# Kernel tuning notes

Measured on AMD Instinct MI355X. Metric: run time of the kernel, lower is better.

Reference implementation:

```python
import jax, jax.numpy as jnp
import numpy as np

PAD = 50
CLUSTERING_WEIGHT = 1.0
SAMPLE_NUMBER = 8192
EPS = 1e-6


def setup_inputs() -> dict:
    key = jax.random.key(0)
    k1, k2 = jax.random.split(key)
    n, c, h, w = 2, 19, 512, 512
    output = jax.random.uniform(k1, (n, c, h, w), dtype=jnp.float32)
    hw_cropped = (h - 2 * PAD) * (w - 2 * PAD)  # 412*412 = 169744
    sample = jax.random.randint(k2, (SAMPLE_NUMBER,), 0, hw_cropped, dtype=jnp.int64)
    return {"output": output, "sample": sample}


def reference(output, sample):
    n, c, h, w = output.shape
    # crop pad border
    out = output[:, :, PAD:h - PAD, PAD:w - PAD]  # [n, c, h', w']
    prob = out.reshape(n, c, -1)[:, :, sample]     # [n, c, S]
    prob_t = jnp.swapaxes(prob, 1, 2)              # [n, S, c]
    # sampled similarity: [n, S, S] (memory-heavy intermediate)
    sim = jnp.einsum('nsc,ntc->nst', prob_t, prob_t)
    ind = jnp.argmax(sim, axis=2)                  # [n, S]
    # nearest[b, i, k] = prob_t[b, ind[b, i], k]
    nearest = jnp.take_along_axis(prob_t, ind[:, :, None], axis=1)  # [n, S, c]
    # robust_crossentropy(pred=prob_t, tgt=nearest)
    loss = -(nearest * jnp.log(prob_t + EPS))
    loss = loss.mean() * CLUSTERING_WEIGHT
    return loss[None]  # shape [1]
```

## Files before the change

### kernel.cpp

```cpp
#include <hip/hip_runtime.h>
#include <math.h>

#define N 2
#define C 19
#define H 512
#define W 512
#define PADC 50
#define WC 412
#define S 8192
#define CP 20
#define XP 64
#define NCHUNK 16
#define CHUNKT (S / NCHUNK)
#define TTS 128
#define NSTG (CHUNKT / TTS)
#define TPS (TTS / 32)
#define LPITCH 72
#define EPSF 1e-6f

typedef __attribute__((ext_vector_type(8))) short short8;
typedef __attribute__((ext_vector_type(16))) float f32x16;

__device__ __forceinline__ unsigned short f2bf_rne(float x) {
    unsigned u = __float_as_uint(x);
    unsigned r = (u + 0x7FFFu + ((u >> 16) & 1u)) >> 16;
    return (unsigned short)r;
}
__device__ __forceinline__ float bf2f(unsigned short h) {
    return __uint_as_float(((unsigned)h) << 16);
}
__device__ __forceinline__ float max16(const f32x16 a) {
    float m0 = fmaxf(a[0], a[1]),   m1 = fmaxf(a[2], a[3]);
    float m2 = fmaxf(a[4], a[5]),   m3 = fmaxf(a[6], a[7]);
    float m4 = fmaxf(a[8], a[9]),   m5 = fmaxf(a[10], a[11]);
    float m6 = fmaxf(a[12], a[13]), m7 = fmaxf(a[14], a[15]);
    m0 = fmaxf(m0, m1); m2 = fmaxf(m2, m3);
    m4 = fmaxf(m4, m5); m6 = fmaxf(m6, m7);
    m0 = fmaxf(m0, m2); m4 = fmaxf(m4, m6);
    return fmaxf(m0, m4);
}

__global__ void gather_k(const float* __restrict__ out4d,
                         const int* __restrict__ sample,
                         float* __restrict__ P32,
                         unsigned short* __restrict__ X) {
    int idx = blockIdx.x * blockDim.x + threadIdx.x;
    int lane = idx & 31;
    int ns = idx >> 5;
    int nn = ns >> 13;
    int s  = ns & (S - 1);
    int smp = sample[s];
    int row = smp / WC;
    int col = smp - row * WC;
    const float* base = out4d + ((size_t)nn * C) * H * W
                      + (size_t)(PADC + row) * W + (PADC + col);
    float v = 0.f;
    if (lane < C) v = base[(size_t)lane * (H * W)];
    unsigned short hb = f2bf_rne(v);
    float hf = bf2f(hb);
    unsigned short lb = f2bf_rne(v - hf);

    if (lane < CP) P32[(size_t)ns * CP + lane] = v;
    unsigned short* xr = X + (size_t)ns * XP;
    xr[lane]      = hb;
    xr[32 + lane] = lb;
}

__global__ __launch_bounds__(512, 4) void argmax_k(const unsigned short* __restrict__ X,
                                                   unsigned* __restrict__ keys) {
    __shared__ unsigned short lds[2][TTS * LPITCH];
    int b = blockIdx.x;
    int chunk  = b & (NCHUNK - 1);
    int sgroup = (b >> 4) & 15;
    int nn     = b >> 8;
    int tid  = threadIdx.x;
    int w    = tid >> 6;
    int lane = tid & 63;
    int col  = lane & 31;
    int hi   = lane >> 5;
    int s0   = (sgroup * 16 + w) * 32;
    int s1   = s0 + 256;
    int t0   = chunk * CHUNKT;
    const unsigned short* Xn = X + (size_t)nn * S * XP;

    short8 bfA[4], bfB[4];
    {
        const unsigned short* ba = Xn + (size_t)(s0 + col) * XP + hi * 8;
        bfA[0] = *(const short8*)(ba);      bfA[1] = *(const short8*)(ba + 16);
        bfA[2] = *(const short8*)(ba + 32); bfA[3] = *(const short8*)(ba + 48);
        const unsigned short* bb = Xn + (size_t)(s1 + col) * XP + hi * 8;
        bfB[0] = *(const short8*)(bb);      bfB[1] = *(const short8*)(bb + 16);
        bfB[2] = *(const short8*)(bb + 32); bfB[3] = *(const short8*)(bb + 48);
    }

    f32x16 zacc = {};
    unsigned kA = 0u, kB = 0u;

    int r0 = tid >> 3, j0 = tid & 7;
    int r1 = r0 + 64;

    {
        const float4* src = (const float4*)(Xn + (size_t)t0 * XP);
        *(float4*)(&lds[0][r0 * LPITCH + j0 * 8]) = src[tid];
        *(float4*)(&lds[0][r1 * LPITCH + j0 * 8]) = src[tid + 512];
    }
    __syncthreads();

    int cur = 0;
    for (int st = 0; st < NSTG; ++st) {
        float4 na, nb;
        if (st + 1 < NSTG) {
            const float4* srcn = (const float4*)(Xn + (size_t)(t0 + (st + 1) * TTS) * XP);
            na = srcn[tid]; nb = srcn[tid + 512];
        }
        const unsigned short* bs = &lds[cur][0];
        #pragma unroll
        for (int ts = 0; ts < TPS; ++ts) {
            const unsigned short* arow = bs + (ts * 32 + col) * LPITCH + hi * 8;
            short8 a0 = *(const short8*)(arow);
            short8 a1 = *(const short8*)(arow + 16);
            short8 a2 = *(const short8*)(arow + 32);
            short8 a3 = *(const short8*)(arow + 48);
            f32x16 accA = __builtin_amdgcn_mfma_f32_32x32x16_bf16(a0, bfA[0], zacc, 0, 0, 0);
            accA = __builtin_amdgcn_mfma_f32_32x32x16_bf16(a1, bfA[1], accA, 0, 0, 0);
            accA = __builtin_amdgcn_mfma_f32_32x32x16_bf16(a0, bfA[2], accA, 0, 0, 0);
            accA = __builtin_amdgcn_mfma_f32_32x32x16_bf16(a1, bfA[3], accA, 0, 0, 0);
            accA = __builtin_amdgcn_mfma_f32_32x32x16_bf16(a2, bfA[0], accA, 0, 0, 0);
            accA = __builtin_amdgcn_mfma_f32_32x32x16_bf16(a3, bfA[1], accA, 0, 0, 0);
            f32x16 accB = __builtin_amdgcn_mfma_f32_32x32x16_bf16(a0, bfB[0], zacc, 0, 0, 0);
            accB = __builtin_amdgcn_mfma_f32_32x32x16_bf16(a1, bfB[1], accB, 0, 0, 0);
            accB = __builtin_amdgcn_mfma_f32_32x32x16_bf16(a0, bfB[2], accB, 0, 0, 0);
            accB = __builtin_amdgcn_mfma_f32_32x32x16_bf16(a1, bfB[3], accB, 0, 0, 0);
            accB = __builtin_amdgcn_mfma_f32_32x32x16_bf16(a2, bfB[0], accB, 0, 0, 0);
            accB = __builtin_amdgcn_mfma_f32_32x32x16_bf16(a3, bfB[1], accB, 0, 0, 0);
            int tile = st * TPS + ts;
            unsigned tb = (unsigned)(63 - tile);
            float mA = fmaxf(max16(accA), 0.f);
            float mB = fmaxf(max16(accB), 0.f);
            unsigned vA = (__float_as_uint(mA) & ~63u) | tb;
            unsigned vB = (__float_as_uint(mB) & ~63u) | tb;
            kA = kA > vA ? kA : vA;
            kB = kB > vB ? kB : vB;
        }
        if (st + 1 < NSTG) {
            *(float4*)(&lds[cur ^ 1][r0 * LPITCH + j0 * 8]) = na;
            *(float4*)(&lds[cur ^ 1][r1 * LPITCH + j0 * 8]) = nb;
        }
        __syncthreads();
        cur ^= 1;
    }

    unsigned oA = __shfl(kA, lane ^ 32, 64);
    unsigned oB = __shfl(kB, lane ^ 32, 64);
    kA = kA > oA ? kA : oA;
    kB = kB > oB ? kB : oB;
    if (lane < 32) {
        size_t basek = ((size_t)nn * NCHUNK + chunk) * S;
        keys[basek + s0 + col] = kA;
        keys[basek + s1 + col] = kB;
    }
}

__global__ __launch_bounds__(256) void refine_k(const float* __restrict__ P32,
                                                const unsigned* __restrict__ keys,
                                                int* __restrict__ ind) {
    int tid = threadIdx.x;
    int wv = blockIdx.x * 4 + (tid >> 6);
    int lane = tid & 63;
    int hi = lane >> 5;
    int l  = lane & 31;
    int ns = wv * 2 + hi;
    int nn = ns >> 13;
    int s  = ns & (S - 1);

    const unsigned* kp = keys + (size_t)nn * NCHUNK * S + s;
    unsigned bk = kp[0]; int bc = 0;
    #pragma unroll
    for (int c = 1; c < NCHUNK; ++c) {
        unsigned k = kp[(size_t)c * S];
        if ((k >> 6) > (bk >> 6)) { bk = k; bc = c; }
    }
    int tile = 63 - (int)(bk & 63u);
    int tbase = bc * CHUNKT + tile * 32;

    const float* Pn = P32 + (size_t)nn * S * CP;
    const float* sr = Pn + (size_t)s * CP;
    const float* tr = Pn + (size_t)(tbase + l) * CP;
    float v = 0.f;
    #pragma unroll
    for (int c = 0; c < C; ++c) v = fmaf(sr[c], tr[c], v);
    int t = tbase + l;
    #pragma unroll
    for (int off = 16; off > 0; off >>= 1) {
        float ov = __shfl_xor(v, off, 32);
        int   ot = __shfl_xor(t, off, 32);
        if (ov > v || (ov == v && ot < t)) { v = ov; t = ot; }
    }
    if (l == 0) ind[ns] = t;
}

__global__ __launch_bounds__(256) void loss_k(const float* __restrict__ P32,
                                              const int* __restrict__ ind,
                                              float* __restrict__ bsum) {
    __shared__ float red[256];
    int idx = blockIdx.x * 256 + threadIdx.x;
    int nn = idx >> 13;
    int s  = idx & (S - 1);
    int bi = ind[idx];

    const float* Pn   = P32 + (size_t)nn * S * CP;
    const float* nrow = Pn + (size_t)bi * CP;
    const float* ps   = Pn + (size_t)s  * CP;
    float acc = 0.f;
    #pragma unroll
    for (int c = 0; c < C; ++c) acc -= nrow[c] * logf(ps[c] + EPSF);

    red[threadIdx.x] = acc;
    __syncthreads();
    for (int off = 128; off > 0; off >>= 1) {
        if (threadIdx.x < off) red[threadIdx.x] += red[threadIdx.x + off];
        __syncthreads();
    }
    if (threadIdx.x == 0) bsum[blockIdx.x] = red[0];
}

__global__ void final_k(const float* __restrict__ bsum, float* __restrict__ out) {
    float t = 0.f;
    for (int i = 0; i < (N * S) / 256; ++i) t += bsum[i];
    out[0] = t / (float)(N * S * C);
}

extern "C" void kernel_launch(void* const* d_in, const int* in_sizes, int n_in,
                              void* d_out, int out_size, void* d_ws, size_t ws_size,
                              hipStream_t stream) {
    const float* out4d  = (const float*)d_in[0];
    const int*   sample = (const int*)d_in[1];

    float*          P32  = (float*)d_ws;
    unsigned short* X    = (unsigned short*)(P32 + (size_t)N * S * CP);
    unsigned*       keys = (unsigned*)(X + (size_t)N * S * XP);
    int*            ind  = (int*)(keys + (size_t)N * NCHUNK * S);
    float*          bsum = (float*)(ind + (size_t)N * S);
    float*          outp = (float*)d_out;

    gather_k<<<(N * S * 32) / 256, 256, 0, stream>>>(out4d, sample, P32, X);
    argmax_k<<<N * 16 * NCHUNK, 512, 0, stream>>>(X, keys);
    refine_k<<<(N * S) / 8, 256, 0, stream>>>(P32, keys, ind);
    loss_k<<<(N * S) / 256, 256, 0, stream>>>(P32, ind, bsum);
    final_k<<<1, 1, 0, stream>>>(bsum, outp);
}
```

Before: 43.06 us.

## Pack split-bf16 operands to halve MFMAs, fuse refine with loss, parallelize final reduce

The gather kernel now writes two asymmetric packed operand layouts, so the hi*hi, hi*lo and lo*hi products of the split-bf16 dot product fit into 4 MFMAs per tile instead of 6. This cuts matrix-core work in the dominant argmax kernel. The refine and loss kernels are merged so the nearest index never goes through global memory, and the single-thread final sum becomes a 256-thread block reduction. The new packing depends on exact channel-slot arithmetic, so any slot mismatch would silently change the similarity values.

```diff
diff --git a/kernel.cpp b/kernel.cpp
--- a/kernel.cpp
+++ b/kernel.cpp
@@ -29,23 +29,26 @@
 __device__ __forceinline__ float bf2f(unsigned short h) {
     return __uint_as_float(((unsigned)h) << 16);
 }
-__device__ __forceinline__ float max16(const f32x16 a) {
-    float m0 = fmaxf(a[0], a[1]),   m1 = fmaxf(a[2], a[3]);
-    float m2 = fmaxf(a[4], a[5]),   m3 = fmaxf(a[6], a[7]);
-    float m4 = fmaxf(a[8], a[9]),   m5 = fmaxf(a[10], a[11]);
-    float m6 = fmaxf(a[12], a[13]), m7 = fmaxf(a[14], a[15]);
-    m0 = fmaxf(m0, m1); m2 = fmaxf(m2, m3);
-    m4 = fmaxf(m4, m5); m6 = fmaxf(m6, m7);
-    m0 = fmaxf(m0, m2); m4 = fmaxf(m4, m6);
-    return fmaxf(m0, m4);
+__device__ __forceinline__ float max16c(const f32x16 a) {
+    float m0 = fmaxf(fmaxf(a[0], a[1]), a[2]);
+    float m1 = fmaxf(fmaxf(a[3], a[4]), a[5]);
+    float m2 = fmaxf(fmaxf(a[6], a[7]), a[8]);
+    float m3 = fmaxf(fmaxf(a[9], a[10]), a[11]);
+    float m4 = fmaxf(fmaxf(a[12], a[13]), a[14]);
+    float n0 = fmaxf(fmaxf(m0, m1), m2);
+    float n1 = fmaxf(fmaxf(m3, m4), a[15]);
+    return fmaxf(fmaxf(n0, n1), 0.f);
 }
 
 __global__ void gather_k(const float* __restrict__ out4d,
                          const int* __restrict__ sample,
                          float* __restrict__ P32,
-                         unsigned short* __restrict__ X) {
+                         unsigned short* __restrict__ XA,
+                         unsigned short* __restrict__ XB) {
     int idx = blockIdx.x * blockDim.x + threadIdx.x;
-    int lane = idx & 31;
+    int lane = idx & 63;
+    int hi   = lane >> 5;
+    int l    = lane & 31;
     int ns = idx >> 5;
     int nn = ns >> 13;
     int s  = ns & (S - 1);
@@ -55,18 +58,35 @@
     const float* base = out4d + ((size_t)nn * C) * H * W
                       + (size_t)(PADC + row) * W + (PADC + col);
     float v = 0.f;
-    if (lane < C) v = base[(size_t)lane * (H * W)];
-    unsigned short hb = f2bf_rne(v);
-    float hf = bf2f(hb);
-    unsigned short lb = f2bf_rne(v - hf);
-
-    if (lane < CP) P32[(size_t)ns * CP + lane] = v;
-    unsigned short* xr = X + (size_t)ns * XP;
-    xr[lane]      = hb;
-    xr[32 + lane] = lb;
-}
-
-__global__ __launch_bounds__(512, 4) void argmax_k(const unsigned short* __restrict__ X,
+    if (l < C) v = base[(size_t)l * (H * W)];
+    unsigned hb = f2bf_rne(v);
+    unsigned lb = f2bf_rne(v - bf2f((unsigned short)hb));
+
+    if (l < CP) P32[(size_t)ns * CP + l] = v;
+
+    int base32 = hi << 5;
+    int srcA = base32 + (l < C ? l : l - C);
+    int srcB = base32 + (l < C ? l : l - 6);
+    unsigned lbA = (unsigned)__shfl((int)lb, srcA, 64);
+    unsigned hbA = (unsigned)__shfl((int)hb, srcA, 64);
+    unsigned lbB = (unsigned)__shfl((int)lb, srcB, 64);
+    unsigned hbB = (unsigned)__shfl((int)hb, srcB, 64);
+
+    unsigned short a0 = (unsigned short)(l < C ? hb : lbA);
+    unsigned short a1 = (unsigned short)(l < C ? hb : (l < 25 ? lbB : 0u));
+    unsigned short b0 = (unsigned short)hbA;
+    unsigned short b1 = (unsigned short)(l < C ? lb : (l < 25 ? hbB : 0u));
+
+    unsigned short* xa = XA + (size_t)ns * XP;
+    unsigned short* xb = XB + (size_t)ns * XP;
+    xa[l]      = a0;
+    xa[32 + l] = a1;
+    xb[l]      = b0;
+    xb[32 + l] = b1;
+}
+
+__global__ __launch_bounds__(512, 4) void argmax_k(const unsigned short* __restrict__ XA,
+                                                   const unsigned short* __restrict__ XB,
                                                    unsigned* __restrict__ keys) {
     __shared__ unsigned short lds[2][TTS * LPITCH];
     int b = blockIdx.x;
@@ -81,14 +101,15 @@
     int s0   = (sgroup * 16 + w) * 32;
     int s1   = s0 + 256;
     int t0   = chunk * CHUNKT;
-    const unsigned short* Xn = X + (size_t)nn * S * XP;
+    const unsigned short* XAn = XA + (size_t)nn * S * XP;
+    const unsigned short* XBn = XB + (size_t)nn * S * XP;
 
     short8 bfA[4], bfB[4];
     {
-        const unsigned short* ba = Xn + (size_t)(s0 + col) * XP + hi * 8;
+        const unsigned short* ba = XBn + (size_t)(s0 + col) * XP + hi * 8;
         bfA[0] = *(const short8*)(ba);      bfA[1] = *(const short8*)(ba + 16);
         bfA[2] = *(const short8*)(ba + 32); bfA[3] = *(const short8*)(ba + 48);
-        const unsigned short* bb = Xn + (size_t)(s1 + col) * XP + hi * 8;
+        const unsigned short* bb = XBn + (size_t)(s1 + col) * XP + hi * 8;
         bfB[0] = *(const short8*)(bb);      bfB[1] = *(const short8*)(bb + 16);
         bfB[2] = *(const short8*)(bb + 32); bfB[3] = *(const short8*)(bb + 48);
     }
@@ -100,7 +121,7 @@
     int r1 = r0 + 64;
 
     {
-        const float4* src = (const float4*)(Xn + (size_t)t0 * XP);
+        const float4* src = (const float4*)(XAn + (size_t)t0 * XP);
         *(float4*)(&lds[0][r0 * LPITCH + j0 * 8]) = src[tid];
         *(float4*)(&lds[0][r1 * LPITCH + j0 * 8]) = src[tid + 512];
     }
@@ -110,7 +131,7 @@
     for (int st = 0; st < NSTG; ++st) {
         float4 na, nb;
         if (st + 1 < NSTG) {
-            const float4* srcn = (const float4*)(Xn + (size_t)(t0 + (st + 1) * TTS) * XP);
+            const float4* srcn = (const float4*)(XAn + (size_t)(t0 + (st + 1) * TTS) * XP);
             na = srcn[tid]; nb = srcn[tid + 512];
         }
         const unsigned short* bs = &lds[cur][0];
@@ -123,22 +144,16 @@
             short8 a3 = *(const short8*)(arow + 48);
             f32x16 accA = __builtin_amdgcn_mfma_f32_32x32x16_bf16(a0, bfA[0], zacc, 0, 0, 0);
             accA = __builtin_amdgcn_mfma_f32_32x32x16_bf16(a1, bfA[1], accA, 0, 0, 0);
-            accA = __builtin_amdgcn_mfma_f32_32x32x16_bf16(a0, bfA[2], accA, 0, 0, 0);
-            accA = __builtin_amdgcn_mfma_f32_32x32x16_bf16(a1, bfA[3], accA, 0, 0, 0);
-            accA = __builtin_amdgcn_mfma_f32_32x32x16_bf16(a2, bfA[0], accA, 0, 0, 0);
-            accA = __builtin_amdgcn_mfma_f32_32x32x16_bf16(a3, bfA[1], accA, 0, 0, 0);
+            accA = __builtin_amdgcn_mfma_f32_32x32x16_bf16(a2, bfA[2], accA, 0, 0, 0);
+            accA = __builtin_amdgcn_mfma_f32_32x32x16_bf16(a3, bfA[3], accA, 0, 0, 0);
             f32x16 accB = __builtin_amdgcn_mfma_f32_32x32x16_bf16(a0, bfB[0], zacc, 0, 0, 0);
             accB = __builtin_amdgcn_mfma_f32_32x32x16_bf16(a1, bfB[1], accB, 0, 0, 0);
-            accB = __builtin_amdgcn_mfma_f32_32x32x16_bf16(a0, bfB[2], accB, 0, 0, 0);
-            accB = __builtin_amdgcn_mfma_f32_32x32x16_bf16(a1, bfB[3], accB, 0, 0, 0);
-            accB = __builtin_amdgcn_mfma_f32_32x32x16_bf16(a2, bfB[0], accB, 0, 0, 0);
-            accB = __builtin_amdgcn_mfma_f32_32x32x16_bf16(a3, bfB[1], accB, 0, 0, 0);
+            accB = __builtin_amdgcn_mfma_f32_32x32x16_bf16(a2, bfB[2], accB, 0, 0, 0);
+            accB = __builtin_amdgcn_mfma_f32_32x32x16_bf16(a3, bfB[3], accB, 0, 0, 0);
             int tile = st * TPS + ts;
             unsigned tb = (unsigned)(63 - tile);
-            float mA = fmaxf(max16(accA), 0.f);
-            float mB = fmaxf(max16(accB), 0.f);
-            unsigned vA = (__float_as_uint(mA) & ~63u) | tb;
-            unsigned vB = (__float_as_uint(mB) & ~63u) | tb;
+            unsigned vA = (__float_as_uint(max16c(accA)) & ~63u) | tb;
+            unsigned vB = (__float_as_uint(max16c(accB)) & ~63u) | tb;
             kA = kA > vA ? kA : vA;
             kB = kB > vB ? kB : vB;
         }
@@ -161,15 +176,15 @@
     }
 }
 
-__global__ __launch_bounds__(256) void refine_k(const float* __restrict__ P32,
-                                                const unsigned* __restrict__ keys,
-                                                int* __restrict__ ind) {
+__global__ __launch_bounds__(256) void refine_loss_k(const float* __restrict__ P32,
+                                                     const unsigned* __restrict__ keys,
+                                                     float* __restrict__ bsum) {
+    __shared__ float red[8];
     int tid = threadIdx.x;
-    int wv = blockIdx.x * 4 + (tid >> 6);
     int lane = tid & 63;
     int hi = lane >> 5;
     int l  = lane & 31;
-    int ns = wv * 2 + hi;
+    int ns = blockIdx.x * 8 + (tid >> 6) * 2 + hi;
     int nn = ns >> 13;
     int s  = ns & (S - 1);
 
@@ -196,38 +211,36 @@
         int   ot = __shfl_xor(t, off, 32);
         if (ov > v || (ov == v && ot < t)) { v = ov; t = ot; }
     }
-    if (l == 0) ind[ns] = t;
-}
-
-__global__ __launch_bounds__(256) void loss_k(const float* __restrict__ P32,
-                                              const int* __restrict__ ind,
-                                              float* __restrict__ bsum) {
+    const float* nrow = Pn + (size_t)t * CP;
+    float term = 0.f;
+    if (l < C) term = -nrow[l] * logf(sr[l] + EPSF);
+    #pragma unroll
+    for (int off = 16; off > 0; off >>= 1)
+        term += __shfl_xor(term, off, 32);
+    if (l == 0) red[tid >> 5] = term;
+    __syncthreads();
+    if (tid == 0) {
+        float a = 0.f;
+        #pragma unroll
+        for (int i = 0; i < 8; ++i) a += red[i];
+        bsum[blockIdx.x] = a;
+    }
+}
+
+__global__ __launch_bounds__(256) void final_k(const float* __restrict__ bsum,
+                                               float* __restrict__ out) {
     __shared__ float red[256];
-    int idx = blockIdx.x * 256 + threadIdx.x;
-    int nn = idx >> 13;
-    int s  = idx & (S - 1);
-    int bi = ind[idx];
-
-    const float* Pn   = P32 + (size_t)nn * S * CP;
-    const float* nrow = Pn + (size_t)bi * CP;
-    const float* ps   = Pn + (size_t)s  * CP;
-    float acc = 0.f;
-    #pragma unroll
-    for (int c = 0; c < C; ++c) acc -= nrow[c] * logf(ps[c] + EPSF);
-
-    red[threadIdx.x] = acc;
+    int tid = threadIdx.x;
+    float a = 0.f;
+    #pragma unroll
+    for (int i = 0; i < 8; ++i) a += bsum[i * 256 + tid];
+    red[tid] = a;
     __syncthreads();
     for (int off = 128; off > 0; off >>= 1) {
-        if (threadIdx.x < off) red[threadIdx.x] += red[threadIdx.x + off];
+        if (tid < off) red[tid] += red[tid + off];
         __syncthreads();
     }
-    if (threadIdx.x == 0) bsum[blockIdx.x] = red[0];
-}
-
-__global__ void final_k(const float* __restrict__ bsum, float* __restrict__ out) {
-    float t = 0.f;
-    for (int i = 0; i < (N * S) / 256; ++i) t += bsum[i];
-    out[0] = t / (float)(N * S * C);
+    if (tid == 0) out[0] = red[0] / (float)(N * S * C);
 }
 
 extern "C" void kernel_launch(void* const* d_in, const int* in_sizes, int n_in,
@@ -237,15 +250,14 @@
     const int*   sample = (const int*)d_in[1];
 
     float*          P32  = (float*)d_ws;
-    unsigned short* X    = (unsigned short*)(P32 + (size_t)N * S * CP);
-    unsigned*       keys = (unsigned*)(X + (size_t)N * S * XP);
-    int*            ind  = (int*)(keys + (size_t)N * NCHUNK * S);
-    float*          bsum = (float*)(ind + (size_t)N * S);
+    unsigned short* XA   = (unsigned short*)(P32 + (size_t)N * S * CP);
+    unsigned short* XB   = XA + (size_t)N * S * XP;
+    unsigned*       keys = (unsigned*)(XB + (size_t)N * S * XP);
+    float*          bsum = (float*)(keys + (size_t)N * NCHUNK * S);
     float*          outp = (float*)d_out;
 
-    gather_k<<<(N * S * 32) / 256, 256, 0, stream>>>(out4d, sample, P32, X);
-    argmax_k<<<N * 16 * NCHUNK, 512, 0, stream>>>(X, keys);
-    refine_k<<<(N * S) / 8, 256, 0, stream>>>(P32, keys, ind);
-    loss_k<<<(N * S) / 256, 256, 0, stream>>>(P32, ind, bsum);
-    final_k<<<1, 1, 0, stream>>>(bsum, outp);
-}
+    gather_k<<<(N * S * 32) / 256, 256, 0, stream>>>(out4d, sample, P32, XA, XB);
+    argmax_k<<<N * 16 * NCHUNK, 512, 0, stream>>>(XA, XB, keys);
+    refine_loss_k<<<(N * S) / 8, 256, 0, stream>>>(P32, keys, bsum);
+    final_k<<<1, 256, 0, stream>>>(bsum, outp);
+}
```

New measurement: 36.20 us. -15.9%, faster.
